# Optimization experiments

Measured on AMD Instinct MI355X. Metric: run time of the kernel, lower is better.

The kernel has to match this reference:

```python
import jax, jax.numpy as jnp
import numpy as np

B, L, D, NH = 4, 1024, 1024, 16
DH = D // NH
H = 8 * D // 3  # SwiGLU hidden = 2730
NEG = -1e9


def setup_inputs() -> dict:
    key = jax.random.key(0)
    ks = jax.random.split(key, 8)
    init = lambda k, shape: (jax.random.normal(k, shape, jnp.float32) * 0.02)
    x = jax.random.normal(ks[0], (B, L, D), jnp.float32)
    causal = jnp.tril(jnp.ones((L, L), bool))
    m = jnp.where(causal, 0.0, NEG)[None, None].astype(jnp.float32)  # [1,1,L,L]
    return {
        'x': x,
        'm': m,
        'wx': init(ks[1], (D, 3 * D)),
        'bx': jnp.zeros((3 * D,), jnp.float32),
        'wo': init(ks[2], (D, D)),
        'bo': jnp.zeros((D,), jnp.float32),
        'mhanorm_w': jnp.ones((D,), jnp.float32),
        'ffnorm_w': jnp.ones((D,), jnp.float32),
        'u': init(ks[3], (D, H)),
        'v': init(ks[4], (D, H)),
        'w': init(ks[5], (H, D)),
    }


def rmsnorm(x, weight, eps=1e-8):
    rrms = jax.lax.rsqrt(jnp.mean(x * x, axis=-1, keepdims=True) + eps)
    return weight * x * rrms


def reference(x, m, wx, bx, wo, bo, mhanorm_w, ffnorm_w, u, v, w):
    scale = D ** (-0.5)  # note: original uses d**-0.5, NOT dh**-0.5
    qkv = rmsnorm(x, mhanorm_w) @ wx + bx                 # [B,L,3D]
    q, k, vv = jnp.split(qkv, 3, axis=-1)                  # each [B,L,D]
    split = lambda t: t.reshape(B, L, NH, DH).transpose(0, 2, 1, 3)  # [B,NH,L,DH]
    q, k, vv = split(q), split(k), split(vv)               # pe = identity (default)
    scores = jnp.einsum('bhic,bhjc->bhij', q, k) * scale + m
    A = jax.nn.softmax(scores, axis=-1)
    head = jnp.einsum('bhij,bhjc->bhic', A, vv)            # [B,NH,L,DH]
    head = head.transpose(0, 2, 1, 3).reshape(B, L, D)
    x = x + head @ wo + bo
    xn = rmsnorm(x, ffnorm_w)
    return x + (jax.nn.silu(xn @ u) * (xn @ v)) @ w
```

## Files before the change

kernel.cpp:

```cpp
#include <hip/hip_runtime.h>

#define B_  4
#define L_  1024
#define D_  1024
#define NH_ 16
#define DH_ 64
#define H_  2730
#define HP_ 2816
#define M_  4096

typedef short bf16x8 __attribute__((ext_vector_type(8)));
typedef float f32x4  __attribute__((ext_vector_type(4)));

__device__ __forceinline__ unsigned short f2bf(float f) {
    unsigned int u = __builtin_bit_cast(unsigned int, f);
    u += 0x7fffu + ((u >> 16) & 1u);
    return (unsigned short)(u >> 16);
}
__device__ __forceinline__ float bf2f(unsigned short s) {
    unsigned int u = ((unsigned int)s) << 16;
    return __builtin_bit_cast(float, u);
}

__device__ __forceinline__ void glds16(const void* g, void* l) {
    __builtin_amdgcn_global_load_lds(
        (const __attribute__((address_space(1))) unsigned int*)g,
        (__attribute__((address_space(3))) unsigned int*)l, 16, 0, 0);
}

__device__ __forceinline__ void xcd_swz(int& lx, int& ly) {
    const int gx = gridDim.x;
    const int flat = blockIdx.x + gx * blockIdx.y;
    const int r = flat & 7, q = flat >> 3;
    lx = q % gx;
    ly = r + 8 * (q / gx);
}

__global__ __launch_bounds__(256) void cvtT_all(
    const float* __restrict__ wx, const float* __restrict__ wo,
    const float* __restrict__ u,  const float* __restrict__ v,
    const float* __restrict__ w,
    unsigned short* __restrict__ wxb, unsigned short* __restrict__ wob,
    unsigned short* __restrict__ ub,  unsigned short* __restrict__ vb,
    unsigned short* __restrict__ wb)
{
    const int id = blockIdx.x;
    const float* in; unsigned short* out;
    int K, N, Kp, gx, base;
    if (id < 3072)      { in = wx; out = wxb; K = 1024; N = 3072; Kp = 1024; gx = 32; base = 0; }
    else if (id < 4096) { in = wo; out = wob; K = 1024; N = 1024; Kp = 1024; gx = 32; base = 3072; }
    else if (id < 6912) { in = u;  out = ub;  K = 1024; N = 2730; Kp = 1024; gx = 32; base = 4096; }
    else if (id < 9728) { in = v;  out = vb;  K = 1024; N = 2730; Kp = 1024; gx = 32; base = 6912; }
    else                { in = w;  out = wb;  K = 2730; N = 1024; Kp = 2816; gx = 88; base = 9728; }
    const int local = id - base;
    const int bx = local % gx, by = local / gx;

    __shared__ float t[32][33];
    const int k0 = bx * 32, n0 = by * 32;
    const int tx = threadIdx.x & 31, ty = threadIdx.x >> 5;
    #pragma unroll
    for (int i = 0; i < 4; ++i) {
        const int k = k0 + ty + i * 8, n = n0 + tx;
        t[ty + i * 8][tx] = (k < K && n < N) ? in[(size_t)k * N + n] : 0.0f;
    }
    __syncthreads();
    #pragma unroll
    for (int i = 0; i < 4; ++i) {
        const int n = n0 + ty + i * 8, k = k0 + tx;
        out[(size_t)n * Kp + k] = f2bf(t[tx][ty + i * 8]);
    }
}

__global__ __launch_bounds__(256) void rmsnorm_kernel(
    const float* __restrict__ x, const float* __restrict__ w,
    unsigned short* __restrict__ out)
{
    const int row = blockIdx.x;
    const int t = threadIdx.x;
    const float4 v = ((const float4*)(x + (size_t)row * 1024))[t];
    float ss = v.x*v.x + v.y*v.y + v.z*v.z + v.w*v.w;
    #pragma unroll
    for (int off = 32; off > 0; off >>= 1) ss += __shfl_down(ss, off);
    __shared__ float red[4];
    if ((t & 63) == 0) red[t >> 6] = ss;
    __syncthreads();
    const float tot = red[0] + red[1] + red[2] + red[3];
    const float rr = rsqrtf(tot * (1.0f / 1024.0f) + 1e-8f);
    const float4 wv = ((const float4*)w)[t];
    ushort4 o;
    o.x = f2bf(v.x * wv.x * rr); o.y = f2bf(v.y * wv.y * rr);
    o.z = f2bf(v.z * wv.z * rr); o.w = f2bf(v.w * wv.w * rr);
    ((ushort4*)(out + (size_t)row * 1024))[t] = o;
}

template<int EPI, int TN>
__global__ __launch_bounds__(256) void gemm_bf16(
    const unsigned short* __restrict__ A, const unsigned short* __restrict__ Bt,
    int M, int N, int K,
    const float* __restrict__ bias, const float* __restrict__ res,
    float* __restrict__ outf, unsigned short* __restrict__ outb)
{
    constexpr int NS = TN / 32;
    constexpr int G  = (TN == 128) ? 4 : 3;
    constexpr int WAIT_G = 0xF70 | G;
    __shared__ __align__(16) unsigned short As[2][128 * 32];
    __shared__ __align__(16) unsigned short Bs[2][TN * 32];
    const int tid = threadIdx.x;
    int lx, ly;
    xcd_swz(lx, ly);
    const int m0 = ly * 128, n0 = lx * TN;
    const int lane = tid & 63, w = tid >> 6;
    const int wm = w >> 1, wn = w & 1;
    const int quad = lane >> 4, l15 = lane & 15;

    f32x4 acc[4][NS] = {};

    const int p0 = w * 64 + lane;
    const int r0 = p0 >> 2, c0 = (p0 & 3) ^ ((r0 >> 1) & 3);
    const int offL0 = p0 * 8, offL1 = 2048 + p0 * 8;

    const unsigned short* Ag0 = A + (size_t)(m0 + r0) * K + c0 * 8;
    const unsigned short* Ag1 = A + (size_t)(m0 + 64 + r0) * K + c0 * 8;
    const unsigned short* Bg0 = Bt + (size_t)(n0 + r0) * K + c0 * 8;
    const unsigned short* Bg1 = Bt + (size_t)(n0 + 64 + r0) * K + c0 * 8;

    auto stage = [&](int kk, int buf) {
        glds16(Ag0 + kk, &As[buf][offL0]);
        glds16(Ag1 + kk, &As[buf][offL1]);
        glds16(Bg0 + kk, &Bs[buf][offL0]);
        if (TN == 128) glds16(Bg1 + kk, &Bs[buf][offL1]);
    };
    auto compute = [&](int buf) {
        bf16x8 af[4], bfr[NS];
        #pragma unroll
        for (int ms = 0; ms < 4; ++ms) {
            const int row = wm * 64 + ms * 16 + l15;
            af[ms] = *(const bf16x8*)&As[buf][row * 32 + ((quad ^ ((row >> 1) & 3)) * 8)];
        }
        #pragma unroll
        for (int ns = 0; ns < NS; ++ns) {
            const int row = wn * (TN / 2) + ns * 16 + l15;
            bfr[ns] = *(const bf16x8*)&Bs[buf][row * 32 + ((quad ^ ((row >> 1) & 3)) * 8)];
        }
        #pragma unroll
        for (int ms = 0; ms < 4; ++ms)
            #pragma unroll
            for (int ns = 0; ns < NS; ++ns)
                acc[ms][ns] = __builtin_amdgcn_mfma_f32_16x16x32_bf16(
                    af[ms], bfr[ns], acc[ms][ns], 0, 0, 0);
    };

    const int nk = K >> 5;
    stage(0, 0);
    for (int i = 0; i < nk; i += 2) {
        if (i + 1 < nk) { stage((i + 1) << 5, 1); __builtin_amdgcn_s_waitcnt(WAIT_G); }
        else            { __builtin_amdgcn_s_waitcnt(0xF70); }
        __builtin_amdgcn_s_barrier();
        compute(0);
        __builtin_amdgcn_s_barrier();
        if (i + 2 < nk) { stage((i + 2) << 5, 0); __builtin_amdgcn_s_waitcnt(WAIT_G); }
        else            { __builtin_amdgcn_s_waitcnt(0xF70); }
        __builtin_amdgcn_s_barrier();
        compute(1);
        __builtin_amdgcn_s_barrier();
    }

    #pragma unroll
    for (int ms = 0; ms < 4; ++ms) {
        #pragma unroll
        for (int r = 0; r < 4; ++r) {
            const int row = m0 + wm * 64 + ms * 16 + quad * 4 + r;
            const size_t ro = (size_t)row * N;
            #pragma unroll
            for (int ns = 0; ns < NS; ++ns) {
                const int col = n0 + wn * (TN / 2) + ns * 16 + l15;
                float v = acc[ms][ns][r];
                if (EPI == 0) {
                    outb[ro + col] = f2bf(v + bias[col]);
                } else if (EPI == 1) {
                    outf[ro + col] = v + bias[col] + res[ro + col];
                } else {
                    outf[ro + col] = v + res[ro + col];
                }
            }
        }
    }
}

__global__ __launch_bounds__(256, 2) void gemm_swiglu(
    const unsigned short* __restrict__ A, const unsigned short* __restrict__ Bu,
    const unsigned short* __restrict__ Bv, unsigned short* __restrict__ g)
{
    constexpr int K = 1024, N = HP_;
    constexpr int WAIT_G = 0xF76;
    __shared__ __align__(16) unsigned short As[2][128 * 32];
    __shared__ __align__(16) unsigned short Us[2][128 * 32];
    __shared__ __align__(16) unsigned short Vs[2][128 * 32];
    const int tid = threadIdx.x;
    int lx, ly;
    xcd_swz(lx, ly);
    const int m0 = ly * 128, n0 = lx * 128;
    const int lane = tid & 63, w = tid >> 6;
    const int wm = w >> 1, wn = w & 1;
    const int quad = lane >> 4, l15 = lane & 15;

    f32x4 au[4][4] = {}, av[4][4] = {};

    const int p0 = w * 64 + lane;
    const int r0 = p0 >> 2, c0 = (p0 & 3) ^ ((r0 >> 1) & 3);
    const int offL0 = p0 * 8, offL1 = 2048 + p0 * 8;

    const unsigned short* Ag0 = A  + (size_t)(m0 + r0) * K + c0 * 8;
    const unsigned short* Ag1 = A  + (size_t)(m0 + 64 + r0) * K + c0 * 8;
    const unsigned short* Ug0 = Bu + (size_t)(n0 + r0) * K + c0 * 8;
    const unsigned short* Ug1 = Bu + (size_t)(n0 + 64 + r0) * K + c0 * 8;
    const unsigned short* Vg0 = Bv + (size_t)(n0 + r0) * K + c0 * 8;
    const unsigned short* Vg1 = Bv + (size_t)(n0 + 64 + r0) * K + c0 * 8;

    auto stage = [&](int kk, int buf) {
        glds16(Ag0 + kk, &As[buf][offL0]);
        glds16(Ag1 + kk, &As[buf][offL1]);
        glds16(Ug0 + kk, &Us[buf][offL0]);
        glds16(Ug1 + kk, &Us[buf][offL1]);
        glds16(Vg0 + kk, &Vs[buf][offL0]);
        glds16(Vg1 + kk, &Vs[buf][offL1]);
    };
    auto compute = [&](int buf) {
        bf16x8 af[4], uf[4], vf[4];
        #pragma unroll
        for (int ms = 0; ms < 4; ++ms) {
            const int row = wm * 64 + ms * 16 + l15;
            af[ms] = *(const bf16x8*)&As[buf][row * 32 + ((quad ^ ((row >> 1) & 3)) * 8)];
        }
        #pragma unroll
        for (int ns = 0; ns < 4; ++ns) {
            const int row = wn * 64 + ns * 16 + l15;
            uf[ns] = *(const bf16x8*)&Us[buf][row * 32 + ((quad ^ ((row >> 1) & 3)) * 8)];
            vf[ns] = *(const bf16x8*)&Vs[buf][row * 32 + ((quad ^ ((row >> 1) & 3)) * 8)];
        }
        #pragma unroll
        for (int ms = 0; ms < 4; ++ms)
            #pragma unroll
            for (int ns = 0; ns < 4; ++ns) {
                au[ms][ns] = __builtin_amdgcn_mfma_f32_16x16x32_bf16(af[ms], uf[ns], au[ms][ns], 0, 0, 0);
                av[ms][ns] = __builtin_amdgcn_mfma_f32_16x16x32_bf16(af[ms], vf[ns], av[ms][ns], 0, 0, 0);
            }
    };

    stage(0, 0);
    for (int i = 0; i < 32; i += 2) {
        if (i + 1 < 32) { stage((i + 1) << 5, 1); __builtin_amdgcn_s_waitcnt(WAIT_G); }
        else            { __builtin_amdgcn_s_waitcnt(0xF70); }
        __builtin_amdgcn_s_barrier();
        compute(0);
        __builtin_amdgcn_s_barrier();
        if (i + 2 < 32) { stage((i + 2) << 5, 0); __builtin_amdgcn_s_waitcnt(WAIT_G); }
        else            { __builtin_amdgcn_s_waitcnt(0xF70); }
        __builtin_amdgcn_s_barrier();
        compute(1);
        __builtin_amdgcn_s_barrier();
    }

    #pragma unroll
    for (int ms = 0; ms < 4; ++ms) {
        #pragma unroll
        for (int r = 0; r < 4; ++r) {
            const int row = m0 + wm * 64 + ms * 16 + quad * 4 + r;
            const size_t ro = (size_t)row * N;
            #pragma unroll
            for (int ns = 0; ns < 4; ++ns) {
                const int col = n0 + wn * 64 + ns * 16 + l15;
                const float uu = au[ms][ns][r];
                const float vv = av[ms][ns][r];
                g[ro + col] = f2bf(uu / (1.0f + __expf(-uu)) * vv);
            }
        }
    }
}

__global__ __launch_bounds__(256) void attn_mfma2_kernel(
    const unsigned short* __restrict__ qkv, unsigned short* __restrict__ hout)
{
    __shared__ __align__(16) unsigned short Qs[2][64 * 72];
    __shared__ __align__(16) unsigned short Ks[2][64 * 64];
    __shared__ __align__(16) unsigned short Vt[2][64 * 72];
    __shared__ __align__(16) unsigned short Ps[64 * 68];

    const int tid = threadIdx.x;
    const int qa = blockIdx.x, h = blockIdx.y, b = blockIdx.z;
    const int qb = 15 - qa;
    const int w = tid >> 6, lane = tid & 63;
    const int quad = lane >> 4, l15 = lane & 15;

    const size_t basek = (size_t)(b * L_) * 3072 + 1024 + h * 64;
    const size_t basev = basek + 1024;

    {
        const int row = tid >> 1, half = tid & 1;
        const int tile = row >> 6, r6 = row & 63;
        const int grow = (tile ? qb : qa) * 64 + r6;
        const unsigned short* gp = qkv + (size_t)(b * L_ + grow) * 3072 + h * 64 + half * 32;
        uint4 a = *(const uint4*)gp;
        uint4 c = *(const uint4*)(gp + 8);
        uint4 d = *(const uint4*)(gp + 16);
        uint4 e = *(const uint4*)(gp + 24);
        unsigned short* dp = &Qs[tile][r6 * 72 + half * 32];
        *(uint4*)dp = a; *(uint4*)(dp + 8) = c; *(uint4*)(dp + 16) = d; *(uint4*)(dp + 24) = e;
    }

    auto stageK = [&](int kt, int buf) {
        #pragma unroll
        for (int i = 0; i < 2; ++i) {
            const int p = i * 256 + tid;
            const int row = p >> 3;
            const int cc = (p & 7) ^ (row & 7);
            glds16(qkv + basek + (size_t)(kt * 64 + row) * 3072 + cc * 8, &Ks[buf][p * 8]);
        }
    };
    const int vkey = (tid & 31) * 2, vdp = tid >> 5;
    auto loadV = [&](int kt, uint4& v0, uint4& v1) {
        const unsigned short* gp = qkv + basev + (size_t)(kt * 64 + vkey) * 3072 + vdp * 8;
        v0 = *(const uint4*)gp;
        v1 = *(const uint4*)(gp + 3072);
    };
    auto writeV = [&](int buf, const uint4& v0, const uint4& v1) {
        union { uint4 u; unsigned short s[8]; } a, c;
        a.u = v0; c.u = v1;
        #pragma unroll
        for (int i = 0; i < 8; ++i) {
            unsigned int pk = (unsigned int)a.s[i] | ((unsigned int)c.s[i] << 16);
            *(unsigned int*)&Vt[buf][(vdp * 8 + i) * 72 + vkey] = pk;
        }
    };

    f32x4 O[4] = {};
    float m4[4], l4[4];
    #pragma unroll
    for (int r = 0; r < 4; ++r) { m4[r] = -1e30f; l4[r] = 0.0f; }

    stageK(0, 0);
    {
        uint4 v0, v1;
        loadV(0, v0, v1);
        writeV(0, v0, v1);
    }
    __syncthreads();

    bf16x8 af[2];
    #pragma unroll
    for (int s = 0; s < 2; ++s)
        af[s] = *(const bf16x8*)&Qs[0][(w * 16 + l15) * 72 + s * 32 + quad * 8];

    int qsel = 0, kt = 0;
    for (int t = 0; t < 17; ++t) {
        const int cb = t & 1, nb = cb ^ 1;
        const bool havenext = (t < 16);
        uint4 nv0, nv1;
        if (havenext) {
            const int ktn = (t + 1 <= qa) ? (t + 1) : (t - qa);
            stageK(ktn, nb);
            loadV(ktn, nv0, nv1);
        }

        bf16x8 bfk[4][2];
        #pragma unroll
        for (int n = 0; n < 4; ++n) {
            const int row = n * 16 + l15;
            #pragma unroll
            for (int s = 0; s < 2; ++s)
                bfk[n][s] = *(const bf16x8*)&Ks[cb][row * 64 + (((s * 4 + quad) ^ (row & 7)) * 8)];
        }
        f32x4 sacc[4] = {};
        #pragma unroll
        for (int n = 0; n < 4; ++n) {
            sacc[n] = __builtin_amdgcn_mfma_f32_16x16x32_bf16(af[0], bfk[n][0], sacc[n], 0, 0, 0);
            sacc[n] = __builtin_amdgcn_mfma_f32_16x16x32_bf16(af[1], bfk[n][1], sacc[n], 0, 0, 0);
        }

        const bool diag = (kt == (qsel ? qb : qa));
        float p[4][4], mx[4];
        #pragma unroll
        for (int r = 0; r < 4; ++r) mx[r] = -1e30f;
        #pragma unroll
        for (int n = 0; n < 4; ++n) {
            const int col = n * 16 + l15;
            #pragma unroll
            for (int r = 0; r < 4; ++r) {
                float v = sacc[n][r] * 0.03125f;
                if (diag && col > (w * 16 + quad * 4 + r)) v = -1e30f;
                p[n][r] = v;
                mx[r] = fmaxf(mx[r], v);
            }
        }
        #pragma unroll
        for (int r = 0; r < 4; ++r) {
            #pragma unroll
            for (int m = 1; m < 16; m <<= 1)
                mx[r] = fmaxf(mx[r], __shfl_xor(mx[r], m));
        }
        float alpha[4], rs[4];
        #pragma unroll
        for (int r = 0; r < 4; ++r) {
            const float mnew = fmaxf(m4[r], mx[r]);
            alpha[r] = __expf(m4[r] - mnew);
            m4[r] = mnew;
            float s0 = 0.0f;
            #pragma unroll
            for (int n = 0; n < 4; ++n) {
                const float e = __expf(p[n][r] - mnew);
                p[n][r] = e;
                s0 += e;
            }
            rs[r] = s0;
        }
        #pragma unroll
        for (int r = 0; r < 4; ++r) {
            #pragma unroll
            for (int m = 1; m < 16; m <<= 1)
                rs[r] += __shfl_xor(rs[r], m);
            l4[r] = l4[r] * alpha[r] + rs[r];
        }
        #pragma unroll
        for (int dn = 0; dn < 4; ++dn)
            #pragma unroll
            for (int r = 0; r < 4; ++r)
                O[dn][r] *= alpha[r];
        #pragma unroll
        for (int n = 0; n < 4; ++n)
            #pragma unroll
            for (int r = 0; r < 4; ++r)
                Ps[(w * 16 + quad * 4 + r) * 68 + n * 16 + l15] = f2bf(p[n][r]);

        if (havenext) writeV(nb, nv0, nv1);

        bf16x8 ap[2], bv[4][2];
        #pragma unroll
        for (int s = 0; s < 2; ++s)
            ap[s] = *(const bf16x8*)&Ps[(w * 16 + l15) * 68 + s * 32 + quad * 8];
        #pragma unroll
        for (int dn = 0; dn < 4; ++dn)
            #pragma unroll
            for (int s = 0; s < 2; ++s)
                bv[dn][s] = *(const bf16x8*)&Vt[cb][(dn * 16 + l15) * 72 + s * 32 + quad * 8];
        #pragma unroll
        for (int dn = 0; dn < 4; ++dn) {
            O[dn] = __builtin_amdgcn_mfma_f32_16x16x32_bf16(ap[0], bv[dn][0], O[dn], 0, 0, 0);
            O[dn] = __builtin_amdgcn_mfma_f32_16x16x32_bf16(ap[1], bv[dn][1], O[dn], 0, 0, 0);
        }

        if (t == qa) {
            #pragma unroll
            for (int r = 0; r < 4; ++r) {
                const float inv = 1.0f / l4[r];
                const int grow = qa * 64 + w * 16 + quad * 4 + r;
                unsigned short* op = hout + (size_t)(b * L_ + grow) * 1024 + h * 64;
                #pragma unroll
                for (int dn = 0; dn < 4; ++dn)
                    op[dn * 16 + l15] = f2bf(O[dn][r] * inv);
            }
            #pragma unroll
            for (int dn = 0; dn < 4; ++dn)
                #pragma unroll
                for (int r = 0; r < 4; ++r) O[dn][r] = 0.0f;
            #pragma unroll
            for (int r = 0; r < 4; ++r) { m4[r] = -1e30f; l4[r] = 0.0f; }
            qsel = 1;
            kt = 0;
            #pragma unroll
            for (int s = 0; s < 2; ++s)
                af[s] = *(const bf16x8*)&Qs[1][(w * 16 + l15) * 72 + s * 32 + quad * 8];
        } else {
            ++kt;
        }
        __syncthreads();
    }

    #pragma unroll
    for (int r = 0; r < 4; ++r) {
        const float inv = 1.0f / l4[r];
        const int grow = qb * 64 + w * 16 + quad * 4 + r;
        unsigned short* op = hout + (size_t)(b * L_ + grow) * 1024 + h * 64;
        #pragma unroll
        for (int dn = 0; dn < 4; ++dn)
            op[dn * 16 + l15] = f2bf(O[dn][r] * inv);
    }
}

extern "C" void kernel_launch(void* const* d_in, const int* in_sizes, int n_in,
                              void* d_out, int out_size, void* d_ws, size_t ws_size,
                              hipStream_t stream)
{
    const float* x   = (const float*)d_in[0];
    const float* wx  = (const float*)d_in[2];
    const float* bx  = (const float*)d_in[3];
    const float* wo  = (const float*)d_in[4];
    const float* bo  = (const float*)d_in[5];
    const float* mhw = (const float*)d_in[6];
    const float* ffw = (const float*)d_in[7];
    const float* u   = (const float*)d_in[8];
    const float* v   = (const float*)d_in[9];
    const float* w   = (const float*)d_in[10];
    float* out = (float*)d_out;

    char* W = (char*)d_ws;
    unsigned short* xn_bf   = (unsigned short*)(W + 0);
    unsigned short* wx_bf   = (unsigned short*)(W + 8388608);
    unsigned short* qkv_bf  = (unsigned short*)(W + 14680064);
    unsigned short* head_bf = (unsigned short*)(W + 39845888);
    unsigned short* wo_bf   = (unsigned short*)(W + 48234496);
    float*          x2      = (float*)(W + 50331648);
    unsigned short* u_bf    = (unsigned short*)(W + 67108864);
    unsigned short* v_bf    = (unsigned short*)(W + 72876032);
    unsigned short* w_bf    = (unsigned short*)(W + 78643200);
    unsigned short* g_bf    = (unsigned short*)(W + 84410368);

    cvtT_all<<<12544, 256, 0, stream>>>(wx, wo, u, v, w,
                                        wx_bf, wo_bf, u_bf, v_bf, w_bf);

    rmsnorm_kernel<<<4096, 256, 0, stream>>>(x, mhw, xn_bf);

    gemm_bf16<0, 128><<<dim3(3072 / 128, 32), 256, 0, stream>>>(
        xn_bf, wx_bf, 4096, 3072, 1024, bx, nullptr, nullptr, qkv_bf);

    attn_mfma2_kernel<<<dim3(8, 16, 4), 256, 0, stream>>>(qkv_bf, head_bf);

    gemm_bf16<1, 64><<<dim3(1024 / 64, 32), 256, 0, stream>>>(
        head_bf, wo_bf, 4096, 1024, 1024, bo, x, x2, nullptr);

    rmsnorm_kernel<<<4096, 256, 0, stream>>>(x2, ffw, xn_bf);

    gemm_swiglu<<<dim3(2816 / 128, 32), 256, 0, stream>>>(xn_bf, u_bf, v_bf, g_bf);

    gemm_bf16<4, 64><<<dim3(1024 / 64, 32), 256, 0, stream>>>(
        g_bf, w_bf, 4096, 1024, 2816, nullptr, x2, out, nullptr);
}
```

Measured before the change: 350.8 us.

## Rewrite SwiGLU GEMM as 8-wave 256x128 tile with triple-buffered A prefetch

Replaces the 4-wave 128x128 SwiGLU up-projection GEMM with an 8-wave, 512-thread kernel covering a 256x128 output tile. A is triple-buffered and U/V double-buffered, with loads issued two k-steps ahead. Each k-step is split into two MFMA half-phases, with the next stage's loads interleaved and s_setprio raised during the MFMA bursts. The aim is better operand reuse per LDS byte and better overlap of global loads with matrix math, at the cost of more LDS, more registers per wave and half as many blocks.

New measurement: 360.5 us. 2.8% more time.

```diff
diff --git a/kernel.cpp b/kernel.cpp
--- a/kernel.cpp
+++ b/kernel.cpp
@@ -187,91 +187,116 @@
     }
 }
 
-__global__ __launch_bounds__(256, 2) void gemm_swiglu(
+__global__ __launch_bounds__(512, 2) void gemm_swiglu8(
     const unsigned short* __restrict__ A, const unsigned short* __restrict__ Bu,
     const unsigned short* __restrict__ Bv, unsigned short* __restrict__ g)
 {
-    constexpr int K = 1024, N = HP_;
-    constexpr int WAIT_G = 0xF76;
-    __shared__ __align__(16) unsigned short As[2][128 * 32];
-    __shared__ __align__(16) unsigned short Us[2][128 * 32];
-    __shared__ __align__(16) unsigned short Vs[2][128 * 32];
+    constexpr int NT = 32;
+    __shared__ __align__(16) unsigned short As_[3][256 * 32];
+    __shared__ __align__(16) unsigned short Us_[2][128 * 32];
+    __shared__ __align__(16) unsigned short Vs_[2][128 * 32];
     const int tid = threadIdx.x;
     int lx, ly;
     xcd_swz(lx, ly);
-    const int m0 = ly * 128, n0 = lx * 128;
+    const int m0 = ly * 256, n0 = lx * 128;
     const int lane = tid & 63, w = tid >> 6;
-    const int wm = w >> 1, wn = w & 1;
+    const int wm = w >> 2, wn = w & 3;
     const int quad = lane >> 4, l15 = lane & 15;
 
-    f32x4 au[4][4] = {}, av[4][4] = {};
-
-    const int p0 = w * 64 + lane;
-    const int r0 = p0 >> 2, c0 = (p0 & 3) ^ ((r0 >> 1) & 3);
-    const int offL0 = p0 * 8, offL1 = 2048 + p0 * 8;
-
-    const unsigned short* Ag0 = A  + (size_t)(m0 + r0) * K + c0 * 8;
-    const unsigned short* Ag1 = A  + (size_t)(m0 + 64 + r0) * K + c0 * 8;
-    const unsigned short* Ug0 = Bu + (size_t)(n0 + r0) * K + c0 * 8;
-    const unsigned short* Ug1 = Bu + (size_t)(n0 + 64 + r0) * K + c0 * 8;
-    const unsigned short* Vg0 = Bv + (size_t)(n0 + r0) * K + c0 * 8;
-    const unsigned short* Vg1 = Bv + (size_t)(n0 + 64 + r0) * K + c0 * 8;
-
-    auto stage = [&](int kk, int buf) {
-        glds16(Ag0 + kk, &As[buf][offL0]);
-        glds16(Ag1 + kk, &As[buf][offL1]);
-        glds16(Ug0 + kk, &Us[buf][offL0]);
-        glds16(Ug1 + kk, &Us[buf][offL1]);
-        glds16(Vg0 + kk, &Vs[buf][offL0]);
-        glds16(Vg1 + kk, &Vs[buf][offL1]);
+    f32x4 au[8][2] = {}, av[8][2] = {};
+
+    const unsigned short* agp0;
+    const unsigned short* agp1;
+    const unsigned short* ugp;
+    const unsigned short* vgp;
+    {
+        const int q0 = tid,      r0_ = q0 >> 2, c0_ = (q0 & 3) ^ ((r0_ >> 1) & 3);
+        const int q1 = 512 + tid, r1_ = q1 >> 2, c1_ = (q1 & 3) ^ ((r1_ >> 1) & 3);
+        agp0 = A + (size_t)(m0 + r0_) * 1024 + c0_ * 8;
+        agp1 = A + (size_t)(m0 + r1_) * 1024 + c1_ * 8;
+        ugp  = Bu + (size_t)(n0 + r0_) * 1024 + c0_ * 8;
+        vgp  = Bv + (size_t)(n0 + r0_) * 1024 + c0_ * 8;
+    }
+    const int dA0 = tid * 8, dA1 = 4096 + tid * 8, dU = tid * 8;
+
+    auto stage = [&](int t, int ba, int bc) {
+        glds16(agp0 + t * 32, &As_[ba][dA0]);
+        glds16(agp1 + t * 32, &As_[ba][dA1]);
+        glds16(ugp + t * 32, &Us_[bc][dU]);
+        glds16(vgp + t * 32, &Vs_[bc][dU]);
     };
-    auto compute = [&](int buf) {
-        bf16x8 af[4], uf[4], vf[4];
-        #pragma unroll
-        for (int ms = 0; ms < 4; ++ms) {
-            const int row = wm * 64 + ms * 16 + l15;
-            af[ms] = *(const bf16x8*)&As[buf][row * 32 + ((quad ^ ((row >> 1) & 3)) * 8)];
-        }
-        #pragma unroll
-        for (int ns = 0; ns < 4; ++ns) {
-            const int row = wn * 64 + ns * 16 + l15;
-            uf[ns] = *(const bf16x8*)&Us[buf][row * 32 + ((quad ^ ((row >> 1) & 3)) * 8)];
-            vf[ns] = *(const bf16x8*)&Vs[buf][row * 32 + ((quad ^ ((row >> 1) & 3)) * 8)];
-        }
-        #pragma unroll
-        for (int ms = 0; ms < 4; ++ms)
-            #pragma unroll
-            for (int ns = 0; ns < 4; ++ns) {
-                au[ms][ns] = __builtin_amdgcn_mfma_f32_16x16x32_bf16(af[ms], uf[ns], au[ms][ns], 0, 0, 0);
-                av[ms][ns] = __builtin_amdgcn_mfma_f32_16x16x32_bf16(af[ms], vf[ns], av[ms][ns], 0, 0, 0);
-            }
-    };
-
-    stage(0, 0);
-    for (int i = 0; i < 32; i += 2) {
-        if (i + 1 < 32) { stage((i + 1) << 5, 1); __builtin_amdgcn_s_waitcnt(WAIT_G); }
-        else            { __builtin_amdgcn_s_waitcnt(0xF70); }
-        __builtin_amdgcn_s_barrier();
-        compute(0);
-        __builtin_amdgcn_s_barrier();
-        if (i + 2 < 32) { stage((i + 2) << 5, 0); __builtin_amdgcn_s_waitcnt(WAIT_G); }
-        else            { __builtin_amdgcn_s_waitcnt(0xF70); }
-        __builtin_amdgcn_s_barrier();
-        compute(1);
-        __builtin_amdgcn_s_barrier();
-    }
-
-    #pragma unroll
-    for (int ms = 0; ms < 4; ++ms) {
+
+    int afo[8], ufo[2];
+    #pragma unroll
+    for (int mr = 0; mr < 8; ++mr) {
+        const int row = wm * 128 + mr * 16 + l15;
+        afo[mr] = row * 32 + ((quad ^ ((row >> 1) & 3)) * 8);
+    }
+    #pragma unroll
+    for (int nr = 0; nr < 2; ++nr) {
+        const int row = wn * 32 + nr * 16 + l15;
+        ufo[nr] = row * 32 + ((quad ^ ((row >> 1) & 3)) * 8);
+    }
+
+    stage(0, 0, 0);
+    stage(1, 1, 1);
+    __builtin_amdgcn_s_waitcnt(0xF74);
+    __builtin_amdgcn_s_barrier();
+
+    int ba = 0;
+    for (int t = 0; t < NT; ++t) {
+        const int c = t & 1;
+        bf16x8 af[4], uf[2], vf[2];
+        #pragma unroll
+        for (int mr = 0; mr < 4; ++mr) af[mr] = *(const bf16x8*)&As_[ba][afo[mr]];
+        #pragma unroll
+        for (int nr = 0; nr < 2; ++nr) {
+            uf[nr] = *(const bf16x8*)&Us_[c][ufo[nr]];
+            vf[nr] = *(const bf16x8*)&Vs_[c][ufo[nr]];
+        }
+        __builtin_amdgcn_s_barrier();
+        __builtin_amdgcn_s_setprio(1);
+        #pragma unroll
+        for (int mr = 0; mr < 4; ++mr)
+            #pragma unroll
+            for (int nr = 0; nr < 2; ++nr) {
+                au[mr][nr] = __builtin_amdgcn_mfma_f32_16x16x32_bf16(af[mr], uf[nr], au[mr][nr], 0, 0, 0);
+                av[mr][nr] = __builtin_amdgcn_mfma_f32_16x16x32_bf16(af[mr], vf[nr], av[mr][nr], 0, 0, 0);
+            }
+        __builtin_amdgcn_s_setprio(0);
+        __builtin_amdgcn_s_barrier();
+        bf16x8 ag[4];
+        #pragma unroll
+        for (int mr = 0; mr < 4; ++mr) ag[mr] = *(const bf16x8*)&As_[ba][afo[mr + 4]];
+        const int bn = (ba == 0) ? 2 : ba - 1;
+        if (t + 2 < NT) stage(t + 2, bn, c);
+        __builtin_amdgcn_s_barrier();
+        __builtin_amdgcn_s_setprio(1);
+        #pragma unroll
+        for (int mr = 0; mr < 4; ++mr)
+            #pragma unroll
+            for (int nr = 0; nr < 2; ++nr) {
+                au[mr + 4][nr] = __builtin_amdgcn_mfma_f32_16x16x32_bf16(ag[mr], uf[nr], au[mr + 4][nr], 0, 0, 0);
+                av[mr + 4][nr] = __builtin_amdgcn_mfma_f32_16x16x32_bf16(ag[mr], vf[nr], av[mr + 4][nr], 0, 0, 0);
+            }
+        __builtin_amdgcn_s_setprio(0);
+        if (t + 2 < NT)      __builtin_amdgcn_s_waitcnt(0xF74);
+        else if (t + 1 < NT) __builtin_amdgcn_s_waitcnt(0xF70);
+        __builtin_amdgcn_s_barrier();
+        ba = (ba == 2) ? 0 : ba + 1;
+    }
+
+    #pragma unroll
+    for (int mr = 0; mr < 8; ++mr) {
         #pragma unroll
         for (int r = 0; r < 4; ++r) {
-            const int row = m0 + wm * 64 + ms * 16 + quad * 4 + r;
-            const size_t ro = (size_t)row * N;
-            #pragma unroll
-            for (int ns = 0; ns < 4; ++ns) {
-                const int col = n0 + wn * 64 + ns * 16 + l15;
-                const float uu = au[ms][ns][r];
-                const float vv = av[ms][ns][r];
+            const int row = m0 + wm * 128 + mr * 16 + quad * 4 + r;
+            const size_t ro = (size_t)row * HP_;
+            #pragma unroll
+            for (int nr = 0; nr < 2; ++nr) {
+                const int col = n0 + wn * 32 + nr * 16 + l15;
+                const float uu = au[mr][nr][r];
+                const float vv = av[mr][nr][r];
                 g[ro + col] = f2bf(uu / (1.0f + __expf(-uu)) * vv);
             }
         }
@@ -529,7 +554,7 @@
 
     rmsnorm_kernel<<<4096, 256, 0, stream>>>(x2, ffw, xn_bf);
 
-    gemm_swiglu<<<dim3(2816 / 128, 32), 256, 0, stream>>>(xn_bf, u_bf, v_bf, g_bf);
+    gemm_swiglu8<<<dim3(2816 / 128, 16), 512, 0, stream>>>(xn_bf, u_bf, v_bf, g_bf);
 
     gemm_bf16<4, 64><<<dim3(1024 / 64, 32), 256, 0, stream>>>(
         g_bf, w_bf, 4096, 1024, 2816, nullptr, x2, out, nullptr);
```
